# Kernel optimization log

Measured on AMD Instinct MI355X. Metric: run time of the kernel, lower is better.

The kernel has to match this reference:

```python
import jax, jax.numpy as jnp
import numpy as np

L, CH, S = 4096, 512, 64
SAMPLE_RATE = 4096.0


def setup_inputs() -> dict:
    key = jax.random.key(0)
    kx, ka, kc = jax.random.split(key, 3)
    x = jax.random.normal(kx, (L, CH), dtype=jnp.float32)
    # original init: lognegA = log(arange(1..S)) broadcast over channels; any real values work
    lognegA = jnp.broadcast_to(jnp.log(jnp.arange(1, S + 1, dtype=jnp.float32)), (CH, S)) \
        + 0.0 * jax.random.normal(ka, (CH, S), dtype=jnp.float32)
    B = jnp.ones((CH, S), dtype=jnp.float32)
    C = 0.01 * jax.random.normal(kc, (CH, S), dtype=jnp.float32)  # nn.initializers.normal() stddev=0.01
    return {"x": x, "lognegA": lognegA, "B": B, "C": C}


def reference(x, lognegA, B, C):
    length = x.shape[0]
    dt = 1.0 / SAMPLE_RATE
    A = -jnp.exp(lognegA)                         # [C, S], strictly negative
    Bd = (jnp.exp(A * dt) - 1.0) * B / A          # discretized B, [C, S]
    # Vandermonde-style kernel: Ak[l, c, s] = exp(l * A[c, s] * dt)
    Ak = jnp.exp(jnp.einsum('l,cs->lcs', jnp.arange(length, dtype=x.dtype), A * dt))
    K = jnp.einsum('cs,lcs->lc', C * Bd, Ak)      # [L, C] per-channel kernel
    # per-channel full causal convolution, truncated to length
    y = jax.vmap(jnp.convolve, in_axes=1, out_axes=1)(x, K)[:length]
    return y
```

## Files before the change

kernel.cpp:

```cpp
#include <hip/hip_runtime.h>


namespace {

constexpr int L_ = 4096;
constexpr int CH_ = 512;
constexpr int S_ = 64;
constexpr float DT = 1.0f / 4096.0f;
constexpr int SC = S_ * CH_;
constexpr int SG = 16;

__global__ void k_params(const float* __restrict__ lognegA,
                         const float* __restrict__ B,
                         const float* __restrict__ C,
                         float* __restrict__ rt, float* __restrict__ wt) {
  const int tid = blockIdx.x * blockDim.x + threadIdx.x;
  const int s = tid >> 9;
  const int c = tid & (CH_ - 1);
  const int i = c * S_ + s;
  const float A = -expf(lognegA[i]);
  const float r = expf(A * DT);
  rt[tid] = r;
  wt[tid] = C[i] * ((r - 1.0f) * B[i] / A);
}

template <int T>
__global__ __launch_bounds__(256) void k_local_s(const float* __restrict__ x,
                                                 const float* __restrict__ rt,
                                                 float* __restrict__ carry) {
  const int lane = threadIdx.x & 63;
  const int g = threadIdx.x >> 6;
  const int k = blockIdx.x >> 3;
  const int c = ((blockIdx.x & 7) << 6) + lane;
  const int s0 = g * SG;

  float r[SG], h[SG];
#pragma unroll
  for (int i = 0; i < SG; ++i) {
    r[i] = rt[(s0 + i) * CH_ + c];
    h[i] = 0.0f;
  }

  const float* xp = x + (size_t)k * T * CH_ + c;
#pragma unroll 8
  for (int l = 0; l < T; ++l) {
    const float xv = xp[l * CH_];
#pragma unroll
    for (int i = 0; i < SG; ++i) h[i] = fmaf(r[i], h[i], xv);
  }

#pragma unroll
  for (int i = 0; i < SG; ++i)
    carry[(size_t)k * SC + (s0 + i) * CH_ + c] = h[i];
}

template <int T, int NC>
__global__ void k_combine(const float* __restrict__ rt,
                          float* __restrict__ carry) {
  const int tid = blockIdx.x * blockDim.x + threadIdx.x;

  float rT = rt[tid];
#pragma unroll
  for (int t = 1; t < T; t <<= 1) rT *= rT;

  constexpr int BATCH = (NC < 32) ? NC : 32;
  float state = 0.0f;
  for (int kb = 0; kb < NC; kb += BATCH) {
    float v[BATCH];
#pragma unroll
    for (int j = 0; j < BATCH; ++j) v[j] = carry[(size_t)(kb + j) * SC + tid];
#pragma unroll
    for (int j = 0; j < BATCH; ++j) {
      const float le = v[j];
      v[j] = state;
      state = fmaf(rT, state, le);
    }
#pragma unroll
    for (int j = 0; j < BATCH; ++j) carry[(size_t)(kb + j) * SC + tid] = v[j];
  }
}

template <int T, bool USE_CARRY>
__global__ __launch_bounds__(256) void k_scan_s(const float* __restrict__ x,
                                                const float* __restrict__ rt,
                                                const float* __restrict__ wt,
                                                const float* __restrict__ carry,
                                                float* __restrict__ y) {
  __shared__ float lds[4][8][64];

  const int lane = threadIdx.x & 63;
  const int g = threadIdx.x >> 6;
  const int k = blockIdx.x >> 3;
  const int cb = (blockIdx.x & 7) << 6;
  const int c = cb + lane;
  const int s0 = g * SG;

  float r[SG], w[SG], h[SG];
#pragma unroll
  for (int i = 0; i < SG; ++i) {
    const int idx = (s0 + i) * CH_ + c;
    r[i] = rt[idx];
    w[i] = wt[idx];
    h[i] = USE_CARRY ? carry[(size_t)k * SC + idx] : 0.0f;
  }

  const float* xp = x + (size_t)k * T * CH_ + c;
  float* yp = y + (size_t)k * T * CH_;

  for (int l = 0; l < T; l += 8) {
    float part[8];
#pragma unroll
    for (int j = 0; j < 8; ++j) {
      const float xv = xp[(l + j) * CH_];
      float a0 = 0, a1 = 0, a2 = 0, a3 = 0;
#pragma unroll
      for (int i = 0; i < SG; i += 4) {
        h[i]     = fmaf(r[i],     h[i],     xv);
        h[i + 1] = fmaf(r[i + 1], h[i + 1], xv);
        h[i + 2] = fmaf(r[i + 2], h[i + 2], xv);
        h[i + 3] = fmaf(r[i + 3], h[i + 3], xv);
        a0 = fmaf(w[i],     h[i],     a0);
        a1 = fmaf(w[i + 1], h[i + 1], a1);
        a2 = fmaf(w[i + 2], h[i + 2], a2);
        a3 = fmaf(w[i + 3], h[i + 3], a3);
      }
      part[j] = (a0 + a1) + (a2 + a3);
    }

#pragma unroll
    for (int j = 0; j < 8; ++j) lds[g][j][lane] = part[j];
    __syncthreads();

#pragma unroll
    for (int p = 0; p < 2; ++p) {
      const int idx = (int)threadIdx.x + p * 256;
      const int j = idx >> 6;
      const int ln = idx & 63;
      const float v = (lds[0][j][ln] + lds[1][j][ln]) +
                      (lds[2][j][ln] + lds[3][j][ln]);
      yp[(size_t)(l + j) * CH_ + cb + ln] = v;
    }
    __syncthreads();
  }
}

template <int T>
void launch_all(const float* x, const float* la, const float* B, const float* C,
                float* ws, float* y, hipStream_t stream) {
  constexpr int NC = L_ / T;
  float* carry = ws;
  float* rt = ws + (size_t)NC * SC;
  float* wt = rt + SC;

  k_params<<<SC / 256, 256, 0, stream>>>(la, B, C, rt, wt);
  if (NC > 1) {
    k_local_s<T><<<NC * 8, 256, 0, stream>>>(x, rt, carry);
    k_combine<T, NC><<<SC / 256, 256, 0, stream>>>(rt, carry);
    k_scan_s<T, true><<<NC * 8, 256, 0, stream>>>(x, rt, wt, carry, y);
  } else {
    k_scan_s<T, false><<<8, 256, 0, stream>>>(x, rt, wt, carry, y);
  }
}

}

extern "C" void kernel_launch(void* const* d_in, const int* in_sizes, int n_in,
                              void* d_out, int out_size, void* d_ws, size_t ws_size,
                              hipStream_t stream) {
  const float* x = (const float*)d_in[0];
  const float* la = (const float*)d_in[1];
  const float* B = (const float*)d_in[2];
  const float* C = (const float*)d_in[3];
  float* y = (float*)d_out;
  float* ws = (float*)d_ws;

  int NC = 128;
  while (NC > 1 &&
         ((size_t)NC * SC + 2 * SC) * sizeof(float) > ws_size) NC >>= 1;

  switch (L_ / NC) {
    case 32:   launch_all<32>(x, la, B, C, ws, y, stream); break;
    case 64:   launch_all<64>(x, la, B, C, ws, y, stream); break;
    case 128:  launch_all<128>(x, la, B, C, ws, y, stream); break;
    case 256:  launch_all<256>(x, la, B, C, ws, y, stream); break;
    case 512:  launch_all<512>(x, la, B, C, ws, y, stream); break;
    case 1024: launch_all<1024>(x, la, B, C, ws, y, stream); break;
    case 2048: launch_all<2048>(x, la, B, C, ws, y, stream); break;
    default:   launch_all<4096>(x, la, B, C, ws, y, stream); break;
  }
}
```

Baseline: 94.00 us.

## Fuse parameter computation into scan kernels and parallelize chunk carry combine

Removes the separate parameter kernel: each scan/local kernel recomputes decay and weight factors from lognegA, B, C with vectorized loads, cutting one launch and the rt/wt round trip. The carry combine becomes a two-level scan, with groups of 16 chunks aggregated in parallel across four warps and an LDS prefix over the groups, in place of a serial 128-step loop per thread. Chunk size is fixed at 64 (64 chunks). In exchange, exp work is repeated in every block, and the load pattern for parameters is strided per channel.

New measurement: 92.91 us. Within noise of the previous version (-1.2%).

```diff
diff --git a/kernel.cpp b/kernel.cpp
--- a/kernel.cpp
+++ b/kernel.cpp
@@ -9,25 +9,51 @@
 constexpr float DT = 1.0f / 4096.0f;
 constexpr int SC = S_ * CH_;
 constexpr int SG = 16;
-
-__global__ void k_params(const float* __restrict__ lognegA,
-                         const float* __restrict__ B,
-                         const float* __restrict__ C,
-                         float* __restrict__ rt, float* __restrict__ wt) {
-  const int tid = blockIdx.x * blockDim.x + threadIdx.x;
-  const int s = tid >> 9;
-  const int c = tid & (CH_ - 1);
-  const int i = c * S_ + s;
-  const float A = -expf(lognegA[i]);
-  const float r = expf(A * DT);
-  rt[tid] = r;
-  wt[tid] = C[i] * ((r - 1.0f) * B[i] / A);
+constexpr int T_ = 64;
+constexpr int NC_ = L_ / T_;
+constexpr int GJ = 16;
+constexpr int NJ = NC_ / GJ;
+
+__device__ __forceinline__ void params16(const float* __restrict__ la,
+                                         const float* __restrict__ Bg,
+                                         const float* __restrict__ Cg,
+                                         int c, int s0, float* r, float* w) {
+  const float4* lap = reinterpret_cast<const float4*>(la + c * S_ + s0);
+  if (w == nullptr) {
+#pragma unroll
+    for (int q = 0; q < 4; ++q) {
+      const float4 v = lap[q];
+      const float a[4] = {v.x, v.y, v.z, v.w};
+#pragma unroll
+      for (int t = 0; t < 4; ++t) {
+        const float A = -expf(a[t]);
+        r[q * 4 + t] = expf(A * DT);
+      }
+    }
+  } else {
+    const float4* bp = reinterpret_cast<const float4*>(Bg + c * S_ + s0);
+    const float4* cp = reinterpret_cast<const float4*>(Cg + c * S_ + s0);
+#pragma unroll
+    for (int q = 0; q < 4; ++q) {
+      const float4 v = lap[q], bb = bp[q], cc = cp[q];
+      const float a[4] = {v.x, v.y, v.z, v.w};
+      const float bv[4] = {bb.x, bb.y, bb.z, bb.w};
+      const float cv[4] = {cc.x, cc.y, cc.z, cc.w};
+#pragma unroll
+      for (int t = 0; t < 4; ++t) {
+        const float A = -expf(a[t]);
+        const float rr = expf(A * DT);
+        r[q * 4 + t] = rr;
+        w[q * 4 + t] = cv[t] * ((rr - 1.0f) * bv[t] / A);
+      }
+    }
+  }
 }
 
 template <int T>
-__global__ __launch_bounds__(256) void k_local_s(const float* __restrict__ x,
-                                                 const float* __restrict__ rt,
-                                                 float* __restrict__ carry) {
+__global__ __launch_bounds__(256) void k_local(const float* __restrict__ x,
+                                               const float* __restrict__ la,
+                                               float* __restrict__ carry) {
   const int lane = threadIdx.x & 63;
   const int g = threadIdx.x >> 6;
   const int k = blockIdx.x >> 3;
@@ -35,11 +61,9 @@
   const int s0 = g * SG;
 
   float r[SG], h[SG];
-#pragma unroll
-  for (int i = 0; i < SG; ++i) {
-    r[i] = rt[(s0 + i) * CH_ + c];
-    h[i] = 0.0f;
-  }
+  params16(la, nullptr, nullptr, c, s0, r, nullptr);
+#pragma unroll
+  for (int i = 0; i < SG; ++i) h[i] = 0.0f;
 
   const float* xp = x + (size_t)k * T * CH_ + c;
 #pragma unroll 8
@@ -49,43 +73,55 @@
     for (int i = 0; i < SG; ++i) h[i] = fmaf(r[i], h[i], xv);
   }
 
-#pragma unroll
-  for (int i = 0; i < SG; ++i)
-    carry[(size_t)k * SC + (s0 + i) * CH_ + c] = h[i];
-}
-
-template <int T, int NC>
-__global__ void k_combine(const float* __restrict__ rt,
-                          float* __restrict__ carry) {
-  const int tid = blockIdx.x * blockDim.x + threadIdx.x;
-
-  float rT = rt[tid];
-#pragma unroll
-  for (int t = 1; t < T; t <<= 1) rT *= rT;
-
-  constexpr int BATCH = (NC < 32) ? NC : 32;
-  float state = 0.0f;
-  for (int kb = 0; kb < NC; kb += BATCH) {
-    float v[BATCH];
-#pragma unroll
-    for (int j = 0; j < BATCH; ++j) v[j] = carry[(size_t)(kb + j) * SC + tid];
-#pragma unroll
-    for (int j = 0; j < BATCH; ++j) {
-      const float le = v[j];
-      v[j] = state;
-      state = fmaf(rT, state, le);
-    }
-#pragma unroll
-    for (int j = 0; j < BATCH; ++j) carry[(size_t)(kb + j) * SC + tid] = v[j];
+  float* cw = carry + (size_t)k * SC + s0 * CH_ + c;
+#pragma unroll
+  for (int i = 0; i < SG; ++i) cw[i * CH_] = h[i];
+}
+
+__global__ __launch_bounds__(256) void k_comb(const float* __restrict__ la,
+                                              float* __restrict__ carry) {
+  __shared__ float aggs[NJ][64];
+  const int p = threadIdx.x & 63;
+  const int j = threadIdx.x >> 6;
+  const int pid = (blockIdx.x << 6) + p;
+  const int s = pid >> 9;
+  const int c = pid & (CH_ - 1);
+
+  const float A = -expf(la[c * S_ + s]);
+  const float rT = expf(A * (DT * (float)T_));
+  float rTG = rT * rT;
+  rTG *= rTG;
+  rTG *= rTG;
+  rTG *= rTG;
+
+  float v[GJ];
+#pragma unroll
+  for (int m = 0; m < GJ; ++m) v[m] = carry[(size_t)(j * GJ + m) * SC + pid];
+
+  float agg = 0.0f;
+#pragma unroll
+  for (int m = 0; m < GJ; ++m) agg = fmaf(rT, agg, v[m]);
+  aggs[j][p] = agg;
+  __syncthreads();
+
+  float G = 0.0f;
+  for (int j2 = 0; j2 < j; ++j2) G = fmaf(rTG, G, aggs[j2][p]);
+
+  float st = G;
+#pragma unroll
+  for (int m = 0; m < GJ; ++m) {
+    carry[(size_t)(j * GJ + m) * SC + pid] = st;
+    st = fmaf(rT, st, v[m]);
   }
 }
 
 template <int T, bool USE_CARRY>
-__global__ __launch_bounds__(256) void k_scan_s(const float* __restrict__ x,
-                                                const float* __restrict__ rt,
-                                                const float* __restrict__ wt,
-                                                const float* __restrict__ carry,
-                                                float* __restrict__ y) {
+__global__ __launch_bounds__(256) void k_scan(const float* __restrict__ x,
+                                              const float* __restrict__ la,
+                                              const float* __restrict__ Bg,
+                                              const float* __restrict__ Cg,
+                                              const float* __restrict__ carry,
+                                              float* __restrict__ y) {
   __shared__ float lds[4][8][64];
 
   const int lane = threadIdx.x & 63;
@@ -96,12 +132,15 @@
   const int s0 = g * SG;
 
   float r[SG], w[SG], h[SG];
-#pragma unroll
-  for (int i = 0; i < SG; ++i) {
-    const int idx = (s0 + i) * CH_ + c;
-    r[i] = rt[idx];
-    w[i] = wt[idx];
-    h[i] = USE_CARRY ? carry[(size_t)k * SC + idx] : 0.0f;
+  params16(la, Bg, Cg, c, s0, r, w);
+
+  if (USE_CARRY) {
+    const float* crd = carry + (size_t)k * SC + s0 * CH_ + c;
+#pragma unroll
+    for (int i = 0; i < SG; ++i) h[i] = crd[i * CH_];
+  } else {
+#pragma unroll
+    for (int i = 0; i < SG; ++i) h[i] = 0.0f;
   }
 
   const float* xp = x + (size_t)k * T * CH_ + c;
@@ -110,8 +149,8 @@
   for (int l = 0; l < T; l += 8) {
     float part[8];
 #pragma unroll
-    for (int j = 0; j < 8; ++j) {
-      const float xv = xp[(l + j) * CH_];
+    for (int jj = 0; jj < 8; ++jj) {
+      const float xv = xp[(l + jj) * CH_];
       float a0 = 0, a1 = 0, a2 = 0, a3 = 0;
 #pragma unroll
       for (int i = 0; i < SG; i += 4) {
@@ -124,41 +163,23 @@
         a2 = fmaf(w[i + 2], h[i + 2], a2);
         a3 = fmaf(w[i + 3], h[i + 3], a3);
       }
-      part[j] = (a0 + a1) + (a2 + a3);
-    }
-
-#pragma unroll
-    for (int j = 0; j < 8; ++j) lds[g][j][lane] = part[j];
+      part[jj] = (a0 + a1) + (a2 + a3);
+    }
+
+#pragma unroll
+    for (int jj = 0; jj < 8; ++jj) lds[g][jj][lane] = part[jj];
     __syncthreads();
 
 #pragma unroll
     for (int p = 0; p < 2; ++p) {
       const int idx = (int)threadIdx.x + p * 256;
-      const int j = idx >> 6;
+      const int jj = idx >> 6;
       const int ln = idx & 63;
-      const float v = (lds[0][j][ln] + lds[1][j][ln]) +
-                      (lds[2][j][ln] + lds[3][j][ln]);
-      yp[(size_t)(l + j) * CH_ + cb + ln] = v;
+      const float vv = (lds[0][jj][ln] + lds[1][jj][ln]) +
+                       (lds[2][jj][ln] + lds[3][jj][ln]);
+      yp[(size_t)(l + jj) * CH_ + cb + ln] = vv;
     }
     __syncthreads();
-  }
-}
-
-template <int T>
-void launch_all(const float* x, const float* la, const float* B, const float* C,
-                float* ws, float* y, hipStream_t stream) {
-  constexpr int NC = L_ / T;
-  float* carry = ws;
-  float* rt = ws + (size_t)NC * SC;
-  float* wt = rt + SC;
-
-  k_params<<<SC / 256, 256, 0, stream>>>(la, B, C, rt, wt);
-  if (NC > 1) {
-    k_local_s<T><<<NC * 8, 256, 0, stream>>>(x, rt, carry);
-    k_combine<T, NC><<<SC / 256, 256, 0, stream>>>(rt, carry);
-    k_scan_s<T, true><<<NC * 8, 256, 0, stream>>>(x, rt, wt, carry, y);
-  } else {
-    k_scan_s<T, false><<<8, 256, 0, stream>>>(x, rt, wt, carry, y);
   }
 }
 
@@ -172,20 +193,14 @@
   const float* B = (const float*)d_in[2];
   const float* C = (const float*)d_in[3];
   float* y = (float*)d_out;
-  float* ws = (float*)d_ws;
-
-  int NC = 128;
-  while (NC > 1 &&
-         ((size_t)NC * SC + 2 * SC) * sizeof(float) > ws_size) NC >>= 1;
-
-  switch (L_ / NC) {
-    case 32:   launch_all<32>(x, la, B, C, ws, y, stream); break;
-    case 64:   launch_all<64>(x, la, B, C, ws, y, stream); break;
-    case 128:  launch_all<128>(x, la, B, C, ws, y, stream); break;
-    case 256:  launch_all<256>(x, la, B, C, ws, y, stream); break;
-    case 512:  launch_all<512>(x, la, B, C, ws, y, stream); break;
-    case 1024: launch_all<1024>(x, la, B, C, ws, y, stream); break;
-    case 2048: launch_all<2048>(x, la, B, C, ws, y, stream); break;
-    default:   launch_all<4096>(x, la, B, C, ws, y, stream); break;
-  }
-}
+  float* carry = (float*)d_ws;
+
+  const size_t need = (size_t)NC_ * SC * sizeof(float);
+  if (ws_size >= need) {
+    k_local<T_><<<NC_ * 8, 256, 0, stream>>>(x, la, carry);
+    k_comb<<<SC / 64, 256, 0, stream>>>(la, carry);
+    k_scan<T_, true><<<NC_ * 8, 256, 0, stream>>>(x, la, B, C, carry, y);
+  } else {
+    k_scan<L_, false><<<8, 256, 0, stream>>>(x, la, B, C, carry, y);
+  }
+}
```
